# Optimization experiments

Measured on AMD Instinct MI355X. Metric: run time of the kernel, lower is better.

Reference implementation:

```python
import jax, jax.numpy as jnp
import numpy as np

B, L, D_MODEL = 2, 2048, 1024
D_INNER, D_STATE, D_CONV, DT_RANK = 2048, 16, 4, 64  # expand=2, dt_rank=ceil(1024/16)


def setup_inputs() -> dict:
    key = jax.random.key(0)
    ks = jax.random.split(key, 12)
    s = lambda k, shape, sc=0.02: jax.random.normal(k, shape, dtype=jnp.float32) * sc
    return {
        "x": jax.random.normal(ks[0], (B, L, D_MODEL), dtype=jnp.float32),
        "norm_w": jnp.ones((D_MODEL,), jnp.float32),
        "norm_b": jnp.zeros((D_MODEL,), jnp.float32),
        "in_proj_w": s(ks[1], (2 * D_INNER, D_MODEL)),
        "conv_w": s(ks[2], (D_INNER, 1, D_CONV), 0.1),
        "conv_b": s(ks[3], (D_INNER,), 0.1),
        "x_proj_w": s(ks[4], (DT_RANK + 2 * D_STATE, D_INNER)),
        "dt_proj_w": s(ks[5], (D_INNER, DT_RANK), 0.1),
        "dt_proj_b": s(ks[6], (D_INNER,), 0.5),
        "A_log": jnp.log(jnp.broadcast_to(jnp.arange(1, D_STATE + 1, dtype=jnp.float32), (D_INNER, D_STATE))),
        "D": jnp.ones((D_INNER,), jnp.float32),
        "out_proj_w": s(ks[7], (D_MODEL, D_INNER)),
    }


def _layernorm(x, w, b, eps=1e-5):
    mu = jnp.mean(x, axis=-1, keepdims=True)
    var = jnp.var(x, axis=-1, keepdims=True)
    return (x - mu) * jax.lax.rsqrt(var + eps) * w + b


def _mamba_forward(x, norm_w, norm_b, in_proj_w, conv_w, conv_b, x_proj_w,
                   dt_proj_w, dt_proj_b, A_log, D, out_proj_w):
    residual = x
    xn = _layernorm(x, norm_w, norm_b)
    # in_proj -> split into x-branch and gate z
    xz = jnp.einsum('bld,ed->ble', xn, in_proj_w)  # [B,L,2*D_INNER]
    xc, z = jnp.split(xz, 2, axis=-1)
    # causal depthwise conv1d over time
    xt = jnp.transpose(xc, (0, 2, 1))  # [B,C,L]
    xt = jnp.pad(xt, ((0, 0), (0, 0), (D_CONV - 1, 0)))
    xt = jax.lax.conv_general_dilated(
        xt, conv_w, window_strides=(1,), padding=[(0, 0)],
        feature_group_count=D_INNER,
        dimension_numbers=('NCH', 'OIH', 'NCH')) + conv_b[None, :, None]
    u = jax.nn.silu(jnp.transpose(xt, (0, 2, 1)))  # [B,L,D_INNER]
    # input-dependent dt, B, C
    x_dbl = jnp.einsum('bld,ed->ble', u, x_proj_w)
    dt, Bm, Cm = jnp.split(x_dbl, [DT_RANK, DT_RANK + D_STATE], axis=-1)
    dt = jax.nn.softplus(jnp.einsum('blr,dr->bld', dt, dt_proj_w) + dt_proj_b)  # [B,L,D_INNER]
    A = -jnp.exp(A_log)  # [D_INNER, D_STATE]

    def step(h, inp):
        dt_t, B_t, C_t, u_t = inp  # [B,Di],[B,Ds],[B,Ds],[B,Di]
        dA = jnp.exp(dt_t[..., None] * A)                       # [B,Di,Ds]
        h = dA * h + (dt_t * u_t)[..., None] * B_t[:, None, :]  # [B,Di,Ds]
        y_t = jnp.einsum('bds,bs->bd', h, C_t)
        return h, y_t

    xs = (jnp.transpose(dt, (1, 0, 2)), jnp.transpose(Bm, (1, 0, 2)),
          jnp.transpose(Cm, (1, 0, 2)), jnp.transpose(u, (1, 0, 2)))
    h0 = jnp.zeros((B, D_INNER, D_STATE), dtype=x.dtype)
    _, ys = jax.lax.scan(step, h0, xs)
    y = jnp.transpose(ys, (1, 0, 2)) + u * D  # [B,L,D_INNER]
    y = y * jax.nn.silu(z)
    out = jnp.einsum('ble,de->bld', y, out_proj_w)
    # dropout in eval mode = identity
    return residual + out


def reference(x, norm_w, norm_b, in_proj_w, conv_w, conv_b, x_proj_w,
              dt_proj_w, dt_proj_b, A_log, D, out_proj_w):
    return _mamba_forward(x, norm_w, norm_b, in_proj_w, conv_w, conv_b, x_proj_w,
                          dt_proj_w, dt_proj_b, A_log, D, out_proj_w)
```

## Files before the change

kernel.cpp:

```cpp
#include <hip/hip_runtime.h>
#include <hip/hip_bf16.h>
#include <math.h>

#define BB 2
#define LL 2048
#define DMODEL 1024
#define DINNER 2048
#define DSTATE 16
#define DTRANK 64
#define NROWS (BB * LL)
#define NC 64
#define CK 32
#define KS 16
#define KCH (DINNER / KS)

typedef __bf16 bf16x8 __attribute__((ext_vector_type(8)));
typedef float  f32x4  __attribute__((ext_vector_type(4)));
typedef __attribute__((address_space(3))) void       as3_void;
typedef const __attribute__((address_space(1))) void as1_cvoid;

__device__ __forceinline__ ushort f2bf(float x) {
    __hip_bfloat16 h = __float2bfloat16(x);
    return *(ushort*)&h;
}
__device__ __forceinline__ float bf2f(ushort u) {
    unsigned int v = ((unsigned int)u) << 16;
    return *(float*)&v;
}

__global__ __launch_bounds__(256) void ln_kernel(const float* __restrict__ x,
                                                 const float* __restrict__ w,
                                                 const float* __restrict__ b,
                                                 __hip_bfloat16* __restrict__ xn) {
    int row = blockIdx.x;
    const float* xr = x + (size_t)row * DMODEL;
    float4 v = reinterpret_cast<const float4*>(xr)[threadIdx.x];
    float s  = v.x + v.y + v.z + v.w;
    float ss = v.x * v.x + v.y * v.y + v.z * v.z + v.w * v.w;
    for (int off = 32; off > 0; off >>= 1) {
        s  += __shfl_down(s, off);
        ss += __shfl_down(ss, off);
    }
    __shared__ float red0[4], red1[4];
    __shared__ float mu_s, rstd_s;
    int lane = threadIdx.x & 63, wv = threadIdx.x >> 6;
    if (lane == 0) { red0[wv] = s; red1[wv] = ss; }
    __syncthreads();
    if (threadIdx.x == 0) {
        float S = red0[0] + red0[1] + red0[2] + red0[3];
        float SS = red1[0] + red1[1] + red1[2] + red1[3];
        float mu = S * (1.0f / DMODEL);
        float var = SS * (1.0f / DMODEL) - mu * mu;
        mu_s = mu;
        rstd_s = rsqrtf(var + 1e-5f);
    }
    __syncthreads();
    float mu = mu_s, rstd = rstd_s;
    float4 wv4 = reinterpret_cast<const float4*>(w)[threadIdx.x];
    float4 bv4 = reinterpret_cast<const float4*>(b)[threadIdx.x];
    ushort4 o;
    o.x = f2bf((v.x - mu) * rstd * wv4.x + bv4.x);
    o.y = f2bf((v.y - mu) * rstd * wv4.y + bv4.y);
    o.z = f2bf((v.z - mu) * rstd * wv4.z + bv4.z);
    o.w = f2bf((v.w - mu) * rstd * wv4.w + bv4.w);
    *reinterpret_cast<ushort4*>((ushort*)xn + (size_t)row * DMODEL + threadIdx.x * 4) = o;
}

__global__ __launch_bounds__(256) void cvt_kernel(const float* __restrict__ in,
                                                  __hip_bfloat16* __restrict__ o) {
    int i = (blockIdx.x * 256 + threadIdx.x) * 4;
    float4 v = *reinterpret_cast<const float4*>(in + i);
    ushort4 p;
    p.x = f2bf(v.x); p.y = f2bf(v.y); p.z = f2bf(v.z); p.w = f2bf(v.w);
    *reinterpret_cast<ushort4*>((ushort*)o + i) = p;
}

template <int EPI>
__global__ __launch_bounds__(256) void gemm_bf16(
    const __hip_bfloat16* __restrict__ A, int lda,
    const __hip_bfloat16* __restrict__ W, int ldw,
    float* __restrict__ C, float* __restrict__ C2, int nsplit, int ldc,
    int K, const float* __restrict__ R) {
    __shared__ ushort As[128][32];
    __shared__ ushort Bs[128][32];
    int tid = threadIdx.x;
    int w = tid >> 6, lane = tid & 63;
    int m0 = blockIdx.y * 128, n0 = blockIdx.x * 128;
    int wr = w >> 1, wc = w & 1;

    int srow = (w << 4) + (lane >> 2);
    int skoff = (lane & 3) << 3;
    const ushort* gA = (const ushort*)A + (size_t)(m0 + srow) * lda + skoff;
    const ushort* gB = (const ushort*)W + (size_t)(n0 + srow) * ldw + skoff;
    char* ldsA0 = (char*)&As[0][0] + w * 1024;
    char* ldsB0 = (char*)&Bs[0][0] + w * 1024;

    f32x4 acc[4][4] = {};
    int frow = (lane & 15);
    int fk   = (lane >> 4) << 3;

    for (int k0 = 0; k0 < K; k0 += 32) {
        __syncthreads();
        __builtin_amdgcn_global_load_lds((as1_cvoid*)(gA + k0),                    (as3_void*)(ldsA0),        16, 0, 0);
        __builtin_amdgcn_global_load_lds((as1_cvoid*)(gA + (size_t)64 * lda + k0), (as3_void*)(ldsA0 + 4096), 16, 0, 0);
        __builtin_amdgcn_global_load_lds((as1_cvoid*)(gB + k0),                    (as3_void*)(ldsB0),        16, 0, 0);
        __builtin_amdgcn_global_load_lds((as1_cvoid*)(gB + (size_t)64 * ldw + k0), (as3_void*)(ldsB0 + 4096), 16, 0, 0);
        __syncthreads();

        bf16x8 af[4], bfr[4];
#pragma unroll
        for (int mi = 0; mi < 4; mi++)
            af[mi] = *(const bf16x8*)&As[wr * 64 + mi * 16 + frow][fk];
#pragma unroll
        for (int ni = 0; ni < 4; ni++)
            bfr[ni] = *(const bf16x8*)&Bs[wc * 64 + ni * 16 + frow][fk];
#pragma unroll
        for (int mi = 0; mi < 4; mi++)
#pragma unroll
            for (int ni = 0; ni < 4; ni++)
                acc[mi][ni] = __builtin_amdgcn_mfma_f32_16x16x32_bf16(
                    af[mi], bfr[ni], acc[mi][ni], 0, 0, 0);
    }

    int crow = (lane >> 4) << 2;
    int ccol = lane & 15;
    bool toz = (EPI == 0) && (n0 >= nsplit);
    int nbase = toz ? (n0 - nsplit) : n0;
#pragma unroll
    for (int mi = 0; mi < 4; mi++) {
#pragma unroll
        for (int ni = 0; ni < 4; ni++) {
#pragma unroll
            for (int r = 0; r < 4; r++) {
                int m = m0 + wr * 64 + mi * 16 + crow + r;
                int n = nbase + wc * 64 + ni * 16 + ccol;
                float v = acc[mi][ni][r];
                if (EPI == 2) v += R[(size_t)m * ldc + n];
                if (toz)
                    ((ushort*)C2)[(size_t)m * ldc + n] = f2bf(v);
                else
                    C[(size_t)m * ldc + n] = v;
            }
        }
    }
}

template <int EPI>
__global__ __launch_bounds__(256) void gemm_kernel(
    const float* __restrict__ A, int lda,
    const float* __restrict__ W, int ldw,
    float* __restrict__ C, int ldc,
    int N, int K,
    const float* __restrict__ bias) {
    __shared__ float As[16][64];
    __shared__ float Ws[16][64];
    int m0 = blockIdx.y * 64;
    int n0 = blockIdx.x * 64;
    int tid = threadIdx.x;
    int tm = tid >> 4, tn = tid & 15;
    int lr = tid >> 2;
    int lk = (tid & 3) << 2;

    float acc[4][4] = {};

    for (int k0 = 0; k0 < K; k0 += 16) {
        float4 av = *reinterpret_cast<const float4*>(A + (size_t)(m0 + lr) * lda + k0 + lk);
        float4 wvv;
        int wn = n0 + lr;
        if (wn < N)
            wvv = *reinterpret_cast<const float4*>(W + (size_t)wn * ldw + k0 + lk);
        else
            wvv = make_float4(0.f, 0.f, 0.f, 0.f);
        __syncthreads();
        As[lk + 0][lr] = av.x; As[lk + 1][lr] = av.y;
        As[lk + 2][lr] = av.z; As[lk + 3][lr] = av.w;
        Ws[lk + 0][lr] = wvv.x; Ws[lk + 1][lr] = wvv.y;
        Ws[lk + 2][lr] = wvv.z; Ws[lk + 3][lr] = wvv.w;
        __syncthreads();
#pragma unroll
        for (int k = 0; k < 16; k++) {
            float4 a = *reinterpret_cast<const float4*>(&As[k][tm << 2]);
            float4 bv = *reinterpret_cast<const float4*>(&Ws[k][tn << 2]);
            float ar[4] = {a.x, a.y, a.z, a.w};
            float br[4] = {bv.x, bv.y, bv.z, bv.w};
#pragma unroll
            for (int i = 0; i < 4; i++)
#pragma unroll
                for (int j = 0; j < 4; j++)
                    acc[i][j] = fmaf(ar[i], br[j], acc[i][j]);
        }
    }
#pragma unroll
    for (int i = 0; i < 4; i++) {
        int m = m0 + (tm << 2) + i;
#pragma unroll
        for (int j = 0; j < 4; j++) {
            int n = n0 + (tn << 2) + j;
            if (n < N) {
                float v = acc[i][j];
                if (EPI == 1) {
                    v += bias[n];
                    v = (v > 20.f) ? v : log1pf(__expf(v));
                    ((ushort*)C)[(size_t)m * ldc + n] = f2bf(v);
                } else {
                    C[(size_t)m * ldc + n] = v;
                }
            }
        }
    }
}

__global__ __launch_bounds__(256) void xp_partial(
    const float* __restrict__ A,
    const float* __restrict__ W,
    float* __restrict__ P) {
    __shared__ float As[16][64];
    __shared__ float Ws[16][64];
    int m0 = blockIdx.y * 64;
    int n0 = blockIdx.x * 64;
    int kbase = blockIdx.z * KCH;
    int tid = threadIdx.x;
    int tm = tid >> 4, tn = tid & 15;
    int lr = tid >> 2;
    int lk = (tid & 3) << 2;

    float acc[4][4] = {};

    for (int k0 = kbase; k0 < kbase + KCH; k0 += 16) {
        float4 av = *reinterpret_cast<const float4*>(A + (size_t)(m0 + lr) * DINNER + k0 + lk);
        float4 wvv;
        int wn = n0 + lr;
        if (wn < 96)
            wvv = *reinterpret_cast<const float4*>(W + (size_t)wn * DINNER + k0 + lk);
        else
            wvv = make_float4(0.f, 0.f, 0.f, 0.f);
        __syncthreads();
        As[lk + 0][lr] = av.x; As[lk + 1][lr] = av.y;
        As[lk + 2][lr] = av.z; As[lk + 3][lr] = av.w;
        Ws[lk + 0][lr] = wvv.x; Ws[lk + 1][lr] = wvv.y;
        Ws[lk + 2][lr] = wvv.z; Ws[lk + 3][lr] = wvv.w;
        __syncthreads();
#pragma unroll
        for (int k = 0; k < 16; k++) {
            float4 a = *reinterpret_cast<const float4*>(&As[k][tm << 2]);
            float4 bv = *reinterpret_cast<const float4*>(&Ws[k][tn << 2]);
            float ar[4] = {a.x, a.y, a.z, a.w};
            float br[4] = {bv.x, bv.y, bv.z, bv.w};
#pragma unroll
            for (int i = 0; i < 4; i++)
#pragma unroll
                for (int j = 0; j < 4; j++)
                    acc[i][j] = fmaf(ar[i], br[j], acc[i][j]);
        }
    }
    float* Pz = P + (size_t)blockIdx.z * NROWS * 96;
#pragma unroll
    for (int i = 0; i < 4; i++) {
        int m = m0 + (tm << 2) + i;
#pragma unroll
        for (int j = 0; j < 4; j++) {
            int n = n0 + (tn << 2) + j;
            if (n < 96)
                Pz[(size_t)m * 96 + n] = acc[i][j];
        }
    }
}

__global__ __launch_bounds__(256) void xp_reduce(
    const float* __restrict__ P, float* __restrict__ xdbl) {
    int i = blockIdx.x * 256 + threadIdx.x;
    float s = 0.f;
#pragma unroll
    for (int z = 0; z < KS; z++)
        s += P[(size_t)z * NROWS * 96 + i];
    xdbl[i] = s;
}

__global__ __launch_bounds__(256) void conv_silu_kernel(
    const float* __restrict__ xc, const float* __restrict__ cw,
    const float* __restrict__ cb, float* __restrict__ u32,
    ushort* __restrict__ u16) {
    int c = blockIdx.x * 256 + threadIdx.x;
    int r = blockIdx.y;
    int l = r & (LL - 1);
    float4 wv = reinterpret_cast<const float4*>(cw)[c];
    const float* p = xc + (size_t)r * DINNER + c;
    float acc = cb[c];
    if (l >= 3) acc = fmaf(p[-3 * DINNER], wv.x, acc);
    if (l >= 2) acc = fmaf(p[-2 * DINNER], wv.y, acc);
    if (l >= 1) acc = fmaf(p[-1 * DINNER], wv.z, acc);
    acc = fmaf(p[0], wv.w, acc);
    float sig = 1.f / (1.f + __expf(-acc));
    float uv = acc * sig;
    u32[(size_t)r * DINNER + c] = uv;
    u16[(size_t)r * DINNER + c] = f2bf(uv);
}

__global__ __launch_bounds__(256) void scan_pass1(
    const ushort* __restrict__ dt16, const ushort* __restrict__ u16,
    const float* __restrict__ xdbl, const float* __restrict__ A_log,
    float* __restrict__ hloc, float* __restrict__ aprod) {
    int bc = blockIdx.x >> 3;
    int b = bc >> 6, c = bc & (NC - 1);
    int d = ((blockIdx.x & 7) << 8) + threadIdx.x;
    float a2[DSTATE];
#pragma unroll
    for (int s = 0; s < DSTATE; s++)
        a2[s] = -__expf(A_log[d * DSTATE + s]) * 1.44269504089f;
    float h[DSTATE], ap[DSTATE];
#pragma unroll
    for (int s = 0; s < DSTATE; s++) { h[s] = 0.f; ap[s] = 1.f; }

    int t0 = c * CK;
    const ushort* dtp = dt16 + ((size_t)b * LL + t0) * DINNER + d;
    const ushort* up  = u16  + ((size_t)b * LL + t0) * DINNER + d;
    const float* xr0  = xdbl + ((size_t)b * LL + t0) * 96;

    for (int t = 0; t < CK; t++) {
        float dtv = bf2f(dtp[(size_t)t * DINNER]);
        float uv  = bf2f(up[(size_t)t * DINNER]);
        float du  = dtv * uv;
        const float* xr = xr0 + t * 96;
#pragma unroll
        for (int s = 0; s < DSTATE; s++) {
            float dA = exp2f(dtv * a2[s]);
            h[s] = fmaf(dA, h[s], du * xr[64 + s]);
            ap[s] *= dA;
        }
    }
    size_t base = ((size_t)bc * DSTATE) * DINNER + d;
#pragma unroll
    for (int s = 0; s < DSTATE; s++) {
        hloc[base + (size_t)s * DINNER]  = h[s];
        aprod[base + (size_t)s * DINNER] = ap[s];
    }
}

__global__ __launch_bounds__(256) void scan_pass2(
    float* __restrict__ hloc, const float* __restrict__ aprod) {
    int idx = blockIdx.x * 256 + threadIdx.x;
    int d = idx & (DINNER - 1);
    int s = (idx >> 11) & (DSTATE - 1);
    int b = idx >> 15;
    float run = 0.f;
    for (int c = 0; c < NC; c++) {
        size_t off = ((size_t)((b * NC + c) * DSTATE + s)) * DINNER + d;
        float hl = hloc[off];
        float ap = aprod[off];
        hloc[off] = run;
        run = fmaf(ap, run, hl);
    }
}

__global__ __launch_bounds__(256) void scan_pass3(
    const ushort* __restrict__ dt16, const ushort* __restrict__ u16,
    const float* __restrict__ xdbl, const ushort* __restrict__ zb,
    const float* __restrict__ A_log, const float* __restrict__ Dp,
    const float* __restrict__ hinit, __hip_bfloat16* __restrict__ y) {
    int bc = blockIdx.x >> 3;
    int b = bc >> 6, c = bc & (NC - 1);
    int d = ((blockIdx.x & 7) << 8) + threadIdx.x;
    float a2[DSTATE];
#pragma unroll
    for (int s = 0; s < DSTATE; s++)
        a2[s] = -__expf(A_log[d * DSTATE + s]) * 1.44269504089f;
    float Dd = Dp[d];
    float h[DSTATE];
    size_t base = ((size_t)bc * DSTATE) * DINNER + d;
#pragma unroll
    for (int s = 0; s < DSTATE; s++) h[s] = hinit[base + (size_t)s * DINNER];

    int t0 = c * CK;
    const ushort* dtp = dt16 + ((size_t)b * LL + t0) * DINNER + d;
    const ushort* up  = u16  + ((size_t)b * LL + t0) * DINNER + d;
    const ushort* zp  = zb   + ((size_t)b * LL + t0) * DINNER + d;
    const float* xr0  = xdbl + ((size_t)b * LL + t0) * 96;
    ushort* yp = (ushort*)y + ((size_t)b * LL + t0) * DINNER + d;

    for (int t = 0; t < CK; t++) {
        float dtv = bf2f(dtp[(size_t)t * DINNER]);
        float uv  = bf2f(up[(size_t)t * DINNER]);
        float du  = dtv * uv;
        const float* xr = xr0 + t * 96;
        float yv = 0.f;
#pragma unroll
        for (int s = 0; s < DSTATE; s++) {
            float dA = exp2f(dtv * a2[s]);
            h[s] = fmaf(dA, h[s], du * xr[64 + s]);
            yv = fmaf(h[s], xr[80 + s], yv);
        }
        float zv = bf2f(zp[(size_t)t * DINNER]);
        float sig = 1.f / (1.f + __expf(-zv));
        yv = (yv + uv * Dd) * (zv * sig);
        yp[(size_t)t * DINNER] = f2bf(yv);
    }
}

extern "C" void kernel_launch(void* const* d_in, const int* in_sizes, int n_in,
                              void* d_out, int out_size, void* d_ws, size_t ws_size,
                              hipStream_t stream) {
    const float* x         = (const float*)d_in[0];
    const float* norm_w    = (const float*)d_in[1];
    const float* norm_b    = (const float*)d_in[2];
    const float* in_proj_w = (const float*)d_in[3];
    const float* conv_w    = (const float*)d_in[4];
    const float* conv_b    = (const float*)d_in[5];
    const float* x_proj_w  = (const float*)d_in[6];
    const float* dt_proj_w = (const float*)d_in[7];
    const float* dt_proj_b = (const float*)d_in[8];
    const float* A_log     = (const float*)d_in[9];
    const float* Dp        = (const float*)d_in[10];
    const float* out_proj_w= (const float*)d_in[11];
    float* out = (float*)d_out;

    float* ws   = (float*)d_ws;
    const size_t NI = (size_t)NROWS * DINNER;
    float* xc    = ws;
    float* zbF   = xc + NI;
    ushort* zb   = (ushort*)zbF;
    float* u32   = zbF + NI / 2;
    ushort* u16  = (ushort*)(u32 + NI);
    ushort* dt16 = (ushort*)(u32 + NI + NI / 2);
    float* xdbl  = u32 + NI + NI / 2 + NI / 2;
    __hip_bfloat16* xnb = (__hip_bfloat16*)(xdbl + (size_t)NROWS * 96);
    __hip_bfloat16* ybb = xnb + (size_t)NROWS * DMODEL;
    __hip_bfloat16* wib = ybb + NI;
    __hip_bfloat16* wob = wib + (size_t)2 * DINNER * DMODEL;
    float* hloc  = xc;
    float* aprod = xc + (size_t)BB * NC * DSTATE * DINNER;
    float* xpp   = xc;

    ln_kernel<<<NROWS, 256, 0, stream>>>(x, norm_w, norm_b, xnb);
    cvt_kernel<<<(2 * DINNER * DMODEL) / 1024, 256, 0, stream>>>(in_proj_w, wib);
    cvt_kernel<<<(DMODEL * DINNER) / 1024, 256, 0, stream>>>(out_proj_w, wob);
    gemm_bf16<0><<<dim3((2 * DINNER) / 128, NROWS / 128), 256, 0, stream>>>(
        xnb, DMODEL, wib, DMODEL, xc, zbF, DINNER, DINNER, DMODEL, nullptr);
    conv_silu_kernel<<<dim3(DINNER / 256, NROWS), 256, 0, stream>>>(
        xc, conv_w, conv_b, u32, u16);
    xp_partial<<<dim3(2, NROWS / 64, KS), 256, 0, stream>>>(u32, x_proj_w, xpp);
    xp_reduce<<<(NROWS * 96) / 256, 256, 0, stream>>>(xpp, xdbl);
    gemm_kernel<1><<<dim3(DINNER / 64, NROWS / 64), 256, 0, stream>>>(
        xdbl, 96, dt_proj_w, DTRANK, (float*)dt16, DINNER, DINNER, DTRANK, dt_proj_b);
    scan_pass1<<<BB * NC * (DINNER / 256), 256, 0, stream>>>(
        dt16, u16, xdbl, A_log, hloc, aprod);
    scan_pass2<<<(BB * DSTATE * DINNER) / 256, 256, 0, stream>>>(hloc, aprod);
    scan_pass3<<<BB * NC * (DINNER / 256), 256, 0, stream>>>(
        dt16, u16, xdbl, zb, A_log, Dp, hloc, ybb);
    gemm_bf16<2><<<dim3(DMODEL / 128, NROWS / 128), 256, 0, stream>>>(
        ybb, DINNER, wob, DINNER, out, nullptr, 1 << 30, DMODEL, DINNER, x);
}
```

Measured before the change: 425.5 us.

## Store conv input and SiLU output in bf16, vectorise conv, swizzle GEMM blocks

The in_proj GEMM now writes the x-branch as bf16 instead of fp32. The conv+SiLU kernel reads bf16 with 8-wide vector loads and writes only a bf16 output, and the x_proj partial GEMM reads that bf16 output instead of an fp32 copy. This removes the fp32 xc and u32 buffers and their traffic. The bf16 GEMM also remaps block IDs so that neighbouring blocks share tiles, which should improve cache reuse. The workspace layout moves the scan and partial buffers into separate regions. The cost is extra precision loss on the conv input and on the x_proj input.

```diff
diff --git a/kernel.cpp b/kernel.cpp
--- a/kernel.cpp
+++ b/kernel.cpp
@@ -16,6 +16,7 @@
 
 typedef __bf16 bf16x8 __attribute__((ext_vector_type(8)));
 typedef float  f32x4  __attribute__((ext_vector_type(4)));
+typedef ushort us8    __attribute__((ext_vector_type(8)));
 typedef __attribute__((address_space(3))) void       as3_void;
 typedef const __attribute__((address_space(1))) void as1_cvoid;
 
@@ -79,13 +80,18 @@
 __global__ __launch_bounds__(256) void gemm_bf16(
     const __hip_bfloat16* __restrict__ A, int lda,
     const __hip_bfloat16* __restrict__ W, int ldw,
-    float* __restrict__ C, float* __restrict__ C2, int nsplit, int ldc,
+    void* __restrict__ C, void* __restrict__ C2, int nsplit, int ldc,
     int K, const float* __restrict__ R) {
     __shared__ ushort As[128][32];
     __shared__ ushort Bs[128][32];
     int tid = threadIdx.x;
     int w = tid >> 6, lane = tid & 63;
-    int m0 = blockIdx.y * 128, n0 = blockIdx.x * 128;
+    int nx = gridDim.x;
+    int id = blockIdx.y * nx + blockIdx.x;
+    int q = (nx * gridDim.y) >> 3;
+    int swz = (id & 7) * q + (id >> 3);
+    int bx = swz % nx, by = swz / nx;
+    int m0 = by * 128, n0 = bx * 128;
     int wr = w >> 1, wc = w & 1;
 
     int srow = (w << 4) + (lane >> 2);
@@ -126,6 +132,7 @@
     int ccol = lane & 15;
     bool toz = (EPI == 0) && (n0 >= nsplit);
     int nbase = toz ? (n0 - nsplit) : n0;
+    ushort* Cu = toz ? (ushort*)C2 : (ushort*)C;
 #pragma unroll
     for (int mi = 0; mi < 4; mi++) {
 #pragma unroll
@@ -135,11 +142,12 @@
                 int m = m0 + wr * 64 + mi * 16 + crow + r;
                 int n = nbase + wc * 64 + ni * 16 + ccol;
                 float v = acc[mi][ni][r];
-                if (EPI == 2) v += R[(size_t)m * ldc + n];
-                if (toz)
-                    ((ushort*)C2)[(size_t)m * ldc + n] = f2bf(v);
-                else
-                    C[(size_t)m * ldc + n] = v;
+                if (EPI == 2) {
+                    v += R[(size_t)m * ldc + n];
+                    ((float*)C)[(size_t)m * ldc + n] = v;
+                } else {
+                    Cu[(size_t)m * ldc + n] = f2bf(v);
+                }
             }
         }
     }
@@ -211,7 +219,7 @@
 }
 
 __global__ __launch_bounds__(256) void xp_partial(
-    const float* __restrict__ A,
+    const ushort* __restrict__ A,
     const float* __restrict__ W,
     float* __restrict__ P) {
     __shared__ float As[16][64];
@@ -227,7 +235,8 @@
     float acc[4][4] = {};
 
     for (int k0 = kbase; k0 < kbase + KCH; k0 += 16) {
-        float4 av = *reinterpret_cast<const float4*>(A + (size_t)(m0 + lr) * DINNER + k0 + lk);
+        ushort4 au = *reinterpret_cast<const ushort4*>(A + (size_t)(m0 + lr) * DINNER + k0 + lk);
+        float4 av = make_float4(bf2f(au.x), bf2f(au.y), bf2f(au.z), bf2f(au.w));
         float4 wvv;
         int wn = n0 + lr;
         if (wn < 96)
@@ -277,23 +286,30 @@
 }
 
 __global__ __launch_bounds__(256) void conv_silu_kernel(
-    const float* __restrict__ xc, const float* __restrict__ cw,
-    const float* __restrict__ cb, float* __restrict__ u32,
-    ushort* __restrict__ u16) {
-    int c = blockIdx.x * 256 + threadIdx.x;
-    int r = blockIdx.y;
+    const ushort* __restrict__ xc16, const float* __restrict__ cw,
+    const float* __restrict__ cb, ushort* __restrict__ u16) {
+    int r = blockIdx.x;
     int l = r & (LL - 1);
-    float4 wv = reinterpret_cast<const float4*>(cw)[c];
-    const float* p = xc + (size_t)r * DINNER + c;
-    float acc = cb[c];
-    if (l >= 3) acc = fmaf(p[-3 * DINNER], wv.x, acc);
-    if (l >= 2) acc = fmaf(p[-2 * DINNER], wv.y, acc);
-    if (l >= 1) acc = fmaf(p[-1 * DINNER], wv.z, acc);
-    acc = fmaf(p[0], wv.w, acc);
-    float sig = 1.f / (1.f + __expf(-acc));
-    float uv = acc * sig;
-    u32[(size_t)r * DINNER + c] = uv;
-    u16[(size_t)r * DINNER + c] = f2bf(uv);
+    int c0 = threadIdx.x << 3;
+    const ushort* base = xc16 + (size_t)r * DINNER + c0;
+    us8 z8 = {0, 0, 0, 0, 0, 0, 0, 0};
+    us8 v0 = *(const us8*)(base);
+    us8 v1 = (l >= 1) ? *(const us8*)(base - DINNER)     : z8;
+    us8 v2 = (l >= 2) ? *(const us8*)(base - 2 * DINNER) : z8;
+    us8 v3 = (l >= 3) ? *(const us8*)(base - 3 * DINNER) : z8;
+    us8 o;
+#pragma unroll
+    for (int j = 0; j < 8; j++) {
+        float4 wj = reinterpret_cast<const float4*>(cw)[c0 + j];
+        float acc = cb[c0 + j];
+        acc = fmaf(bf2f(v3[j]), wj.x, acc);
+        acc = fmaf(bf2f(v2[j]), wj.y, acc);
+        acc = fmaf(bf2f(v1[j]), wj.z, acc);
+        acc = fmaf(bf2f(v0[j]), wj.w, acc);
+        float sig = 1.f / (1.f + __expf(-acc));
+        o[j] = f2bf(acc * sig);
+    }
+    *(us8*)(u16 + (size_t)r * DINNER + c0) = o;
 }
 
 __global__ __launch_bounds__(256) void scan_pass1(
@@ -415,29 +431,26 @@
 
     float* ws   = (float*)d_ws;
     const size_t NI = (size_t)NROWS * DINNER;
-    float* xc    = ws;
-    float* zbF   = xc + NI;
-    ushort* zb   = (ushort*)zbF;
-    float* u32   = zbF + NI / 2;
-    ushort* u16  = (ushort*)(u32 + NI);
-    ushort* dt16 = (ushort*)(u32 + NI + NI / 2);
-    float* xdbl  = u32 + NI + NI / 2 + NI / 2;
+    ushort* xc16 = (ushort*)ws;
+    ushort* zb   = (ushort*)(ws + NI / 2);
+    ushort* u16  = (ushort*)(ws + NI);
+    ushort* dt16 = (ushort*)(ws + NI + NI / 2);
+    float*  xdbl = ws + 2 * NI;
     __hip_bfloat16* xnb = (__hip_bfloat16*)(xdbl + (size_t)NROWS * 96);
     __hip_bfloat16* ybb = xnb + (size_t)NROWS * DMODEL;
     __hip_bfloat16* wib = ybb + NI;
     __hip_bfloat16* wob = wib + (size_t)2 * DINNER * DMODEL;
-    float* hloc  = xc;
-    float* aprod = xc + (size_t)BB * NC * DSTATE * DINNER;
-    float* xpp   = xc;
+    float* hloc  = (float*)(wob + (size_t)DMODEL * DINNER);
+    float* aprod = hloc + NI / 2;
+    float* xpp   = aprod + NI / 2;
 
     ln_kernel<<<NROWS, 256, 0, stream>>>(x, norm_w, norm_b, xnb);
     cvt_kernel<<<(2 * DINNER * DMODEL) / 1024, 256, 0, stream>>>(in_proj_w, wib);
     cvt_kernel<<<(DMODEL * DINNER) / 1024, 256, 0, stream>>>(out_proj_w, wob);
     gemm_bf16<0><<<dim3((2 * DINNER) / 128, NROWS / 128), 256, 0, stream>>>(
-        xnb, DMODEL, wib, DMODEL, xc, zbF, DINNER, DINNER, DMODEL, nullptr);
-    conv_silu_kernel<<<dim3(DINNER / 256, NROWS), 256, 0, stream>>>(
-        xc, conv_w, conv_b, u32, u16);
-    xp_partial<<<dim3(2, NROWS / 64, KS), 256, 0, stream>>>(u32, x_proj_w, xpp);
+        xnb, DMODEL, wib, DMODEL, xc16, zb, DINNER, DINNER, DMODEL, nullptr);
+    conv_silu_kernel<<<NROWS, 256, 0, stream>>>(xc16, conv_w, conv_b, u16);
+    xp_partial<<<dim3(2, NROWS / 64, KS), 256, 0, stream>>>(u16, x_proj_w, xpp);
     xp_reduce<<<(NROWS * 96) / 256, 256, 0, stream>>>(xpp, xdbl);
     gemm_kernel<1><<<dim3(DINNER / 64, NROWS / 64), 256, 0, stream>>>(
         xdbl, 96, dt_proj_w, DTRANK, (float*)dt16, DINNER, DINNER, DTRANK, dt_proj_b);
```

Result: no change. 420.4 us (-1.2%).
